# Optimization experiments

Hardware: AMD Instinct MI355X
Metric: run time of the kernel (lower is better)

The kernel has to match this reference:

```python
import jax, jax.numpy as jnp
import numpy as np

N, E = 50000, 800000
NODE_DIM, EDGE_DIM, TIME_DIM, OUT_DIM, N_HEADS = 128, 64, 16, 128, 4
IN_DIM = NODE_DIM + EDGE_DIM + TIME_DIM  # msg_proj input


def setup_inputs() -> dict:
    key = jax.random.key(0)
    ks = jax.random.split(key, 8)
    x = jax.random.normal(ks[0], (N, NODE_DIM), dtype=jnp.float32)
    edge_index = jax.random.randint(ks[1], (2, E), 0, N, dtype=jnp.int32)
    edge_feat = jax.random.normal(ks[2], (E, EDGE_DIM), dtype=jnp.float32)
    time_deltas = jax.random.uniform(ks[3], (E,), dtype=jnp.float32)
    # parameters
    gammas = jnp.ones((TIME_DIM,), jnp.float32)  # ExponentialTimeDecay init_gamma=1.0
    Wm = 0.02 * jax.random.normal(ks[4], (IN_DIM, OUT_DIM), dtype=jnp.float32)
    bm = jnp.zeros((OUT_DIM,), jnp.float32)
    Wa = 0.02 * jax.random.normal(ks[5], (2 * OUT_DIM, N_HEADS), dtype=jnp.float32)
    ba = jnp.zeros((N_HEADS,), jnp.float32)
    Wo = 0.02 * jax.random.normal(ks[6], (OUT_DIM + NODE_DIM, OUT_DIM), dtype=jnp.float32)
    bo = jnp.zeros((OUT_DIM,), jnp.float32)
    ln_g = jnp.ones((OUT_DIM,), jnp.float32)
    ln_b = jnp.zeros((OUT_DIM,), jnp.float32)
    return {"x": x, "edge_index": edge_index, "edge_feat": edge_feat,
            "time_deltas": time_deltas, "gammas": gammas, "Wm": Wm, "bm": bm,
            "Wa": Wa, "ba": ba, "Wo": Wo, "bo": bo, "ln_g": ln_g, "ln_b": ln_b}


def reference(x, edge_index, edge_feat, time_deltas, gammas, Wm, bm, Wa, ba, Wo, bo, ln_g, ln_b):
    src, dst = edge_index[0], edge_index[1]
    # exponential time decay encoding: (E, TIME_DIM)
    dt = jnp.clip(time_deltas, 0.0)[:, None]
    time_enc = jnp.exp(-jax.nn.softplus(gammas)[None, :] * dt)
    # gather + project messages: (E, OUT_DIM)
    msg_in = jnp.concatenate([x[src], edge_feat, time_enc], axis=-1)
    msgs = msg_in @ Wm + bm
    # edge attention, softmax over ALL edges (dim=0, as in the torch code)
    attn_in = jnp.concatenate([msgs, x[dst]], axis=-1)  # (E, 2*OUT_DIM)
    attn_logits = attn_in @ Wa + ba                      # (E, N_HEADS)
    attn_weight = jnp.mean(jax.nn.softmax(attn_logits, axis=0), axis=-1, keepdims=True)
    weighted = msgs * attn_weight
    # scatter-add into per-node aggregates: (N, OUT_DIM)
    agg = jax.ops.segment_sum(weighted, dst, num_segments=N)
    # output MLP (dropout is identity in eval) + LayerNorm
    out = jax.nn.gelu(jnp.concatenate([agg, x], axis=-1) @ Wo + bo, approximate=False)
    mu = jnp.mean(out, axis=-1, keepdims=True)
    var = jnp.mean((out - mu) ** 2, axis=-1, keepdims=True)
    return (out - mu) / jnp.sqrt(var + 1e-5) * ln_g + ln_b
```

## Files before the change

kernel.cpp:

```cpp
#include <hip/hip_runtime.h>
#include <math.h>

#define N_NODES 50000
#define N_EDGES 800000
#define ND 128
#define ED 64
#define TD 16
#define OD 128
#define NH 4
#define INDIM 208
#define K2DIM 336
#define KPAD 352
#define WTPITCH 360
#define NPAD 50048

#define OFF_A      0ll
#define OFF_EXPL   0ll
#define OFF_PERM   8808448ll
#define OFF_DENOM  12008448ll
#define OFF_SPG    12008464ll
#define OFF_WFUSE  12008480ll
#define OFF_BFUSE  12009312ll
#define OFF_BMO    12009328ll
#define OFF_XS4    12009456ll
#define OFF_XD4    12209456ll
#define OFF_CNT    12409456ll
#define OFF_START  12459456ll
#define OFF_CURSOR 12509472ll
#define OFF_SW     12559472ll
#define OFF_WT     12609520ll
#define WS_FLOATS  12632560ll

typedef __attribute__((ext_vector_type(8))) short short8v;
typedef __attribute__((ext_vector_type(4))) float f32x4;

__device__ inline unsigned short f2bf(float f) {
  unsigned u = __float_as_uint(f);
  unsigned r = (u + 0x7fffu + ((u >> 16) & 1u)) >> 16;
  return (unsigned short)r;
}

__global__ void k0_prep(const float* __restrict__ Wm, const float* __restrict__ bm,
                        const float* __restrict__ Wa, const float* __restrict__ ba,
                        const float* __restrict__ Wo, const float* __restrict__ gammas,
                        float* __restrict__ ws) {
  int b = blockIdx.x, j = threadIdx.x;
  unsigned short* Wt = (unsigned short*)(ws + OFF_WT);
  if (b < INDIM) {
    float acc = 0.f;
    for (int m = 0; m < OD; ++m) acc += Wm[b * OD + m] * Wo[m * OD + j];
    Wt[j * WTPITCH + b] = f2bf(acc);
    if (j < NH) {
      float a = 0.f;
      for (int m = 0; m < OD; ++m) a += Wm[b * OD + m] * Wa[m * NH + j];
      ws[OFF_WFUSE + (long)b * NH + j] = a;
    }
  } else if (b < K2DIM) {
    Wt[j * WTPITCH + b] = f2bf(Wo[(OD + b - INDIM) * OD + j]);
  } else {
    if (j < TD) ws[OFF_SPG + j] = log1pf(expf(gammas[j]));
    if (j < NH) {
      float a = ba[j];
      for (int m = 0; m < OD; ++m) a += bm[m] * Wa[m * NH + j];
      ws[OFF_BFUSE + j] = a;
    }
    float a2 = 0.f;
    for (int m = 0; m < OD; ++m) a2 += bm[m] * Wo[m * OD + j];
    ws[OFF_BMO + j] = a2;
    for (int p = K2DIM; p < KPAD; ++p) Wt[j * WTPITCH + p] = 0;
  }
}

__global__ __launch_bounds__(256) void k0b_nodeproj(
    const float* __restrict__ x, const float* __restrict__ Wa,
    float* __restrict__ ws) {
  __shared__ float wf[ND * NH];
  __shared__ float wab[ND * NH];
  int tid = threadIdx.x;
  for (int i = tid; i < ND * NH; i += 256) { wf[i] = ws[OFF_WFUSE + i]; wab[i] = Wa[ND * NH + i]; }
  __syncthreads();
  int lane = tid & 63, wv = tid >> 6;
  long n = (long)blockIdx.x * 4 + wv;
  if (n >= N_NODES) return;
  float v0 = x[n * ND + lane], v1 = x[n * ND + 64 + lane];
  float s0, s1, s2, s3, d0, d1, d2, d3;
  s0 = v0 * wf[lane * 4 + 0] + v1 * wf[(64 + lane) * 4 + 0];
  s1 = v0 * wf[lane * 4 + 1] + v1 * wf[(64 + lane) * 4 + 1];
  s2 = v0 * wf[lane * 4 + 2] + v1 * wf[(64 + lane) * 4 + 2];
  s3 = v0 * wf[lane * 4 + 3] + v1 * wf[(64 + lane) * 4 + 3];
  d0 = v0 * wab[lane * 4 + 0] + v1 * wab[(64 + lane) * 4 + 0];
  d1 = v0 * wab[lane * 4 + 1] + v1 * wab[(64 + lane) * 4 + 1];
  d2 = v0 * wab[lane * 4 + 2] + v1 * wab[(64 + lane) * 4 + 2];
  d3 = v0 * wab[lane * 4 + 3] + v1 * wab[(64 + lane) * 4 + 3];
  for (int off = 32; off; off >>= 1) {
    s0 += __shfl_xor(s0, off); s1 += __shfl_xor(s1, off);
    s2 += __shfl_xor(s2, off); s3 += __shfl_xor(s3, off);
    d0 += __shfl_xor(d0, off); d1 += __shfl_xor(d1, off);
    d2 += __shfl_xor(d2, off); d3 += __shfl_xor(d3, off);
  }
  if (lane == 0) {
    reinterpret_cast<float4*>(ws + OFF_XS4)[n] = make_float4(s0, s1, s2, s3);
    reinterpret_cast<float4*>(ws + OFF_XD4)[n] = make_float4(d0, d1, d2, d3);
  }
}

__global__ __launch_bounds__(256) void k1_logits(
    const int* __restrict__ ei, const float* __restrict__ ef,
    const float* __restrict__ td, float* __restrict__ ws) {
  __shared__ float wef[ED * NH];
  __shared__ float wte[TD * NH];
  __shared__ float bf[NH];
  __shared__ float spg[TD];
  __shared__ float part[NH];
  int tid = threadIdx.x;
  for (int i = tid; i < ED * NH; i += 256) wef[i] = ws[OFF_WFUSE + ND * NH + i];
  if (tid < TD * NH) wte[tid] = ws[OFF_WFUSE + (ND + ED) * NH + tid];
  if (tid < NH) { bf[tid] = ws[OFF_BFUSE + tid]; part[tid] = 0.f; }
  if (tid < TD) spg[tid] = ws[OFF_SPG + tid];
  __syncthreads();

  int r = tid & 15;
  long grp = ((long)blockIdx.x * 256 + tid) >> 4;
  long ngrp = ((long)gridDim.x * 256) >> 4;
  const float4* ef4 = reinterpret_cast<const float4*>(ef);
  float4* expl4 = reinterpret_cast<float4*>(ws + OFF_EXPL);
  const float4* xs4 = reinterpret_cast<const float4*>(ws + OFF_XS4);
  const float4* xd4 = reinterpret_cast<const float4*>(ws + OFF_XD4);
  int* cnt = reinterpret_cast<int*>(ws + OFF_CNT);
  float p0 = 0.f, p1 = 0.f, p2 = 0.f, p3 = 0.f;

  for (long e = grp; e < N_EDGES; e += ngrp) {
    float4 efv = ef4[e * 16 + r];
    const float* w0 = &wef[(4 * r) * 4];
    float a0 = efv.x * w0[0] + efv.y * w0[4] + efv.z * w0[8]  + efv.w * w0[12];
    float a1 = efv.x * w0[1] + efv.y * w0[5] + efv.z * w0[9]  + efv.w * w0[13];
    float a2 = efv.x * w0[2] + efv.y * w0[6] + efv.z * w0[10] + efv.w * w0[14];
    float a3 = efv.x * w0[3] + efv.y * w0[7] + efv.z * w0[11] + efv.w * w0[15];
    float dt = fmaxf(td[e], 0.f);
    float te = expf(-spg[r] * dt);
    a0 += te * wte[r * 4 + 0]; a1 += te * wte[r * 4 + 1];
    a2 += te * wte[r * 4 + 2]; a3 += te * wte[r * 4 + 3];
    for (int off = 8; off; off >>= 1) {
      a0 += __shfl_xor(a0, off); a1 += __shfl_xor(a1, off);
      a2 += __shfl_xor(a2, off); a3 += __shfl_xor(a3, off);
    }
    if (r == 0) {
      int s = ei[e], d = ei[N_EDGES + e];
      float4 xs = xs4[s], xd = xd4[d];
      float e0 = expf(a0 + xs.x + xd.x + bf[0]);
      float e1 = expf(a1 + xs.y + xd.y + bf[1]);
      float e2 = expf(a2 + xs.z + xd.z + bf[2]);
      float e3 = expf(a3 + xs.w + xd.w + bf[3]);
      expl4[e] = make_float4(e0, e1, e2, e3);
      p0 += e0; p1 += e1; p2 += e2; p3 += e3;
      atomicAdd(&cnt[d], 1);
    }
  }
  if ((tid & 15) == 0) {
    atomicAdd(&part[0], p0); atomicAdd(&part[1], p1);
    atomicAdd(&part[2], p2); atomicAdd(&part[3], p3);
  }
  __syncthreads();
  if (tid < NH) atomicAdd(&ws[OFF_DENOM + tid], part[tid]);
}

__global__ __launch_bounds__(1024) void k_scan(float* __restrict__ ws) {
  const int* cnt = reinterpret_cast<const int*>(ws + OFF_CNT);
  int* startp = reinterpret_cast<int*>(ws + OFF_START);
  int* cursor = reinterpret_cast<int*>(ws + OFF_CURSOR);
  __shared__ int wsum[16];
  int tid = threadIdx.x;
  int lo = tid * 49, hi = min(lo + 49, N_NODES);
  int s = 0;
  for (int i = lo; i < hi; ++i) s += cnt[i];
  int lane = tid & 63, wv = tid >> 6;
  int sc = s;
  for (int off = 1; off < 64; off <<= 1) {
    int t = __shfl_up(sc, off);
    if (lane >= off) sc += t;
  }
  if (lane == 63) wsum[wv] = sc;
  __syncthreads();
  if (tid == 0) {
    int run = 0;
    for (int i = 0; i < 16; ++i) { int t = wsum[i]; wsum[i] = run; run += t; }
  }
  __syncthreads();
  int run = wsum[wv] + sc - s;
  for (int i = lo; i < hi; ++i) { startp[i] = run; cursor[i] = run; run += cnt[i]; }
  if (tid == 1023) startp[N_NODES] = run;
}

__global__ __launch_bounds__(256) void k_fill(const int* __restrict__ ei,
                                              const float* __restrict__ td,
                                              float* __restrict__ ws) {
  __shared__ float inv[NH];
  int tid = threadIdx.x;
  if (tid < NH) inv[tid] = 0.25f / ws[OFF_DENOM + tid];
  __syncthreads();
  const float4* expl4 = reinterpret_cast<const float4*>(ws + OFF_EXPL);
  int* cursor = reinterpret_cast<int*>(ws + OFF_CURSOR);
  uint4* perm = reinterpret_cast<uint4*>(ws + OFF_PERM);
  for (long e = (long)blockIdx.x * 256 + tid; e < N_EDGES; e += (long)gridDim.x * 256) {
    int s = ei[e], d = ei[N_EDGES + e];
    float4 ev = expl4[e];
    float w = ev.x * inv[0] + ev.y * inv[1] + ev.z * inv[2] + ev.w * inv[3];
    float dt = fmaxf(td[e], 0.f);
    int pos = atomicAdd(&cursor[d], 1);
    perm[pos] = make_uint4((unsigned)s, (unsigned)e, __float_as_uint(w), __float_as_uint(dt));
  }
}

__global__ __launch_bounds__(256) void k4a_agg(
    const float* __restrict__ x, const float* __restrict__ ef,
    float* __restrict__ ws) {
  __shared__ float spg_s[TD];
  int tid = threadIdx.x;
  if (tid < TD) spg_s[tid] = ws[OFF_SPG + tid];
  __syncthreads();
  int lane = tid & 63;
  long wid = (long)blockIdx.x * 4 + (tid >> 6);
  long nw = (long)gridDim.x * 4;
  const int* start = reinterpret_cast<const int*>(ws + OFF_START);
  const uint4* perm = reinterpret_cast<const uint4*>(ws + OFF_PERM);
  unsigned short* A = (unsigned short*)(ws + OFF_A);
  float spg_l = spg_s[lane & 15];

  for (long n = wid; n < N_NODES; n += nw) {
    int i0 = start[n], i1 = start[n + 1];
    float a0 = 0.f, a1 = 0.f, a2 = 0.f, a3 = 0.f, asw = 0.f;
    for (int base = i0; base < i1; base += 64) {
      int m = min(64, i1 - base);
      uint4 pk = make_uint4(0u, 0u, 0u, 0u);
      if (lane < m) pk = perm[base + lane];
      for (int j = 0; j < m; ++j) {
        int s  = __shfl((int)pk.x, j);
        int e  = __shfl((int)pk.y, j);
        float w  = __uint_as_float(__shfl((int)pk.z, j));
        float dt = __uint_as_float(__shfl((int)pk.w, j));
        a0 += w * x[(long)s * ND + lane];
        a1 += w * x[(long)s * ND + 64 + lane];
        a2 += w * ef[(long)e * ED + lane];
        a3 += w * __expf(-spg_l * dt);
        asw += w;
      }
    }
    unsigned short* Ar = A + n * KPAD;
    float xv0 = x[n * ND + lane], xv1 = x[n * ND + 64 + lane];
    Ar[lane] = f2bf(a0);
    Ar[64 + lane] = f2bf(a1);
    Ar[128 + lane] = f2bf(a2);
    if (lane < TD) Ar[192 + lane] = f2bf(a3);
    Ar[INDIM + lane] = f2bf(xv0);
    Ar[INDIM + 64 + lane] = f2bf(xv1);
    if (lane < 16) Ar[K2DIM + lane] = 0;
    if (lane == 0) ws[OFF_SW + n] = asw;
  }
}

__global__ __launch_bounds__(256) void k4b_mlp(
    const float* __restrict__ bo, const float* __restrict__ lng,
    const float* __restrict__ lnb, const float* __restrict__ ws,
    float* __restrict__ out) {
  __shared__ unsigned short wt[128 * WTPITCH];
  __shared__ float tbl[512];
  int tid = threadIdx.x;
  {
    const unsigned* wg = (const unsigned*)(ws + OFF_WT);
    unsigned* wl = (unsigned*)wt;
    for (int i = tid; i < 128 * WTPITCH / 2; i += 256) wl[i] = wg[i];
    if (tid < 128) {
      tbl[tid] = bo[tid];
      tbl[128 + tid] = ws[OFF_BMO + tid];
      tbl[256 + tid] = lng[tid];
      tbl[384 + tid] = lnb[tid];
    }
  }
  __syncthreads();

  int lane = tid & 63, wv = tid >> 6;
  int c0 = lane & 15, grp = lane >> 4;
  long n0 = (long)blockIdx.x * 64 + (long)wv * 16;
  const unsigned short* A = (const unsigned short*)(ws + OFF_A);
  const unsigned short* Arow = A + (n0 + c0) * KPAD;

  f32x4 acc[8];
#pragma unroll
  for (int t = 0; t < 8; ++t) acc[t] = (f32x4){0.f, 0.f, 0.f, 0.f};

#pragma unroll
  for (int kt = 0; kt < 11; ++kt) {
    short8v afrag = *reinterpret_cast<const short8v*>(Arow + kt * 32 + grp * 8);
#pragma unroll
    for (int t = 0; t < 8; ++t) {
      short8v bfrag = *reinterpret_cast<const short8v*>(&wt[(t * 16 + c0) * WTPITCH + kt * 32 + grp * 8]);
      acc[t] = __builtin_amdgcn_mfma_f32_16x16x32_bf16(afrag, bfrag, acc[t], 0, 0, 0);
    }
  }

  const float* swp = ws + OFF_SW;
  float res[4][8];
#pragma unroll
  for (int r = 0; r < 4; ++r) {
    long row = n0 + grp * 4 + r;
    float sw = swp[row];
    float s = 0.f, s2 = 0.f;
#pragma unroll
    for (int t = 0; t < 8; ++t) {
      int col = c0 + 16 * t;
      float a = acc[t][r] + tbl[col] + sw * tbl[128 + col];
      float h = 0.5f * a * (1.f + erff(a * 0.70710678118654752f));
      res[r][t] = h;
      s += h; s2 += h * h;
    }
    s += __shfl_xor(s, 1);  s2 += __shfl_xor(s2, 1);
    s += __shfl_xor(s, 2);  s2 += __shfl_xor(s2, 2);
    s += __shfl_xor(s, 4);  s2 += __shfl_xor(s2, 4);
    s += __shfl_xor(s, 8);  s2 += __shfl_xor(s2, 8);
    float mu = s * (1.f / 128.f);
    float var = s2 * (1.f / 128.f) - mu * mu;
    float rstd = rsqrtf(var + 1e-5f);
    if (row < N_NODES) {
      float* op = out + row * OD;
#pragma unroll
      for (int t = 0; t < 8; ++t) {
        int col = c0 + 16 * t;
        op[col] = (res[r][t] - mu) * rstd * tbl[256 + col] + tbl[384 + col];
      }
    }
  }
}

extern "C" void kernel_launch(void* const* d_in, const int* in_sizes, int n_in,
                              void* d_out, int out_size, void* d_ws, size_t ws_size,
                              hipStream_t stream) {
  const float* x   = (const float*)d_in[0];
  const int*   ei  = (const int*)d_in[1];
  const float* ef  = (const float*)d_in[2];
  const float* td  = (const float*)d_in[3];
  const float* gm  = (const float*)d_in[4];
  const float* Wm  = (const float*)d_in[5];
  const float* bm  = (const float*)d_in[6];
  const float* Wa  = (const float*)d_in[7];
  const float* ba  = (const float*)d_in[8];
  const float* Wo  = (const float*)d_in[9];
  const float* bo  = (const float*)d_in[10];
  const float* lng = (const float*)d_in[11];
  const float* lnb = (const float*)d_in[12];
  float* ws = (float*)d_ws;
  float* out = (float*)d_out;
  if (ws_size < (size_t)WS_FLOATS * 4) return;

  hipMemsetAsync(ws + OFF_CNT, 0, 50000 * 4, stream);
  hipMemsetAsync(ws + OFF_DENOM, 0, 64, stream);

  k0_prep<<<K2DIM + 1, 128, 0, stream>>>(Wm, bm, Wa, ba, Wo, gm, ws);
  k0b_nodeproj<<<12500, 256, 0, stream>>>(x, Wa, ws);
  k1_logits<<<1024, 256, 0, stream>>>(ei, ef, td, ws);
  k_scan<<<1, 1024, 0, stream>>>(ws);
  k_fill<<<1024, 256, 0, stream>>>(ei, td, ws);
  k4a_agg<<<2048, 256, 0, stream>>>(x, ef, ws);
  k4b_mlp<<<(NPAD / 64), 256, 0, stream>>>(bo, lng, lnb, ws, out);
}
```

Baseline: 455.3 us.

## Restructure edge logits to 4 edges per wave and batch gather loads

The logits kernel now handles four edges per 64-lane wave, with weights held in registers. Every lane does useful work: it issues its own index, time and node-projection loads and uses a transposed shuffle reduction instead of the 16-lane butterfly with a single active writer. The aggregation loop is unrolled by four so the independent x and edge-feature gathers can be in flight together, raising memory-level parallelism. Grid sizes for the logits and fill kernels are doubled. The cost is higher register pressure and the use of the approximate __expf in the logits kernel.

```diff
diff --git a/kernel.cpp b/kernel.cpp
--- a/kernel.cpp
+++ b/kernel.cpp
@@ -119,47 +119,54 @@
   if (tid < TD) spg[tid] = ws[OFF_SPG + tid];
   __syncthreads();
 
-  int r = tid & 15;
-  long grp = ((long)blockIdx.x * 256 + tid) >> 4;
-  long ngrp = ((long)gridDim.x * 256) >> 4;
+  int lane = tid & 63;
+  int q = lane >> 4, r = lane & 15, h = r & 3;
+  long wid = ((long)blockIdx.x * 256 + tid) >> 6;
+  long stride = (long)gridDim.x * 16;
   const float4* ef4 = reinterpret_cast<const float4*>(ef);
-  float4* expl4 = reinterpret_cast<float4*>(ws + OFF_EXPL);
-  const float4* xs4 = reinterpret_cast<const float4*>(ws + OFF_XS4);
-  const float4* xd4 = reinterpret_cast<const float4*>(ws + OFF_XD4);
+  float* expl = ws + OFF_EXPL;
+  const float* xsf = ws + OFF_XS4;
+  const float* xdf = ws + OFF_XD4;
   int* cnt = reinterpret_cast<int*>(ws + OFF_CNT);
-  float p0 = 0.f, p1 = 0.f, p2 = 0.f, p3 = 0.f;
-
-  for (long e = grp; e < N_EDGES; e += ngrp) {
+
+  float wr[16];
+#pragma unroll
+  for (int i = 0; i < 16; ++i) wr[i] = wef[16 * r + i];
+  float spg_r = spg[r];
+  float wt0 = wte[r * 4 + 0], wt1 = wte[r * 4 + 1];
+  float wt2 = wte[r * 4 + 2], wt3 = wte[r * 4 + 3];
+  float bfh = bf[h];
+  float p = 0.f;
+
+  for (long e = wid * 4 + q; e < N_EDGES; e += stride) {
+    int s = ei[e];
+    int d = ei[N_EDGES + e];
+    float dt = fmaxf(td[e], 0.f);
     float4 efv = ef4[e * 16 + r];
-    const float* w0 = &wef[(4 * r) * 4];
-    float a0 = efv.x * w0[0] + efv.y * w0[4] + efv.z * w0[8]  + efv.w * w0[12];
-    float a1 = efv.x * w0[1] + efv.y * w0[5] + efv.z * w0[9]  + efv.w * w0[13];
-    float a2 = efv.x * w0[2] + efv.y * w0[6] + efv.z * w0[10] + efv.w * w0[14];
-    float a3 = efv.x * w0[3] + efv.y * w0[7] + efv.z * w0[11] + efv.w * w0[15];
-    float dt = fmaxf(td[e], 0.f);
-    float te = expf(-spg[r] * dt);
-    a0 += te * wte[r * 4 + 0]; a1 += te * wte[r * 4 + 1];
-    a2 += te * wte[r * 4 + 2]; a3 += te * wte[r * 4 + 3];
-    for (int off = 8; off; off >>= 1) {
-      a0 += __shfl_xor(a0, off); a1 += __shfl_xor(a1, off);
-      a2 += __shfl_xor(a2, off); a3 += __shfl_xor(a3, off);
-    }
-    if (r == 0) {
-      int s = ei[e], d = ei[N_EDGES + e];
-      float4 xs = xs4[s], xd = xd4[d];
-      float e0 = expf(a0 + xs.x + xd.x + bf[0]);
-      float e1 = expf(a1 + xs.y + xd.y + bf[1]);
-      float e2 = expf(a2 + xs.z + xd.z + bf[2]);
-      float e3 = expf(a3 + xs.w + xd.w + bf[3]);
-      expl4[e] = make_float4(e0, e1, e2, e3);
-      p0 += e0; p1 += e1; p2 += e2; p3 += e3;
-      atomicAdd(&cnt[d], 1);
-    }
-  }
-  if ((tid & 15) == 0) {
-    atomicAdd(&part[0], p0); atomicAdd(&part[1], p1);
-    atomicAdd(&part[2], p2); atomicAdd(&part[3], p3);
-  }
+    float ls = xsf[4l * s + h];
+    float ld = xdf[4l * d + h];
+    float te = __expf(-spg_r * dt);
+    float a0 = efv.x * wr[0] + efv.y * wr[4] + efv.z * wr[8]  + efv.w * wr[12] + te * wt0;
+    float a1 = efv.x * wr[1] + efv.y * wr[5] + efv.z * wr[9]  + efv.w * wr[13] + te * wt1;
+    float a2 = efv.x * wr[2] + efv.y * wr[6] + efv.z * wr[10] + efv.w * wr[14] + te * wt2;
+    float a3 = efv.x * wr[3] + efv.y * wr[7] + efv.z * wr[11] + efv.w * wr[15] + te * wt3;
+    a0 += __shfl_xor(a0, 1); a1 += __shfl_xor(a1, 1);
+    a2 += __shfl_xor(a2, 1); a3 += __shfl_xor(a3, 1);
+    a0 += __shfl_xor(a0, 2); a1 += __shfl_xor(a1, 2);
+    a2 += __shfl_xor(a2, 2); a3 += __shfl_xor(a3, 2);
+    float v = a0;
+    v = (h == 1) ? a1 : v;
+    v = (h == 2) ? a2 : v;
+    v = (h == 3) ? a3 : v;
+    v += __shfl_xor(v, 4);
+    v += __shfl_xor(v, 8);
+    float ev = __expf(v + ls + ld + bfh);
+    if (r < 4) { expl[e * 4 + r] = ev; p += ev; }
+    if (r == 1) atomicAdd(&cnt[d], 1);
+  }
+  p += __shfl_xor(p, 16);
+  p += __shfl_xor(p, 32);
+  if (lane < 4) atomicAdd(&part[lane], p);
   __syncthreads();
   if (tid < NH) atomicAdd(&ws[OFF_DENOM + tid], part[tid]);
 }
@@ -233,7 +240,33 @@
       int m = min(64, i1 - base);
       uint4 pk = make_uint4(0u, 0u, 0u, 0u);
       if (lane < m) pk = perm[base + lane];
-      for (int j = 0; j < m; ++j) {
+      int j = 0;
+      for (; j + 4 <= m; j += 4) {
+        int s4[4], e4[4]; float w4[4], dt4[4];
+#pragma unroll
+        for (int u = 0; u < 4; ++u) {
+          s4[u]  = __shfl((int)pk.x, j + u);
+          e4[u]  = __shfl((int)pk.y, j + u);
+          w4[u]  = __uint_as_float(__shfl((int)pk.z, j + u));
+          dt4[u] = __uint_as_float(__shfl((int)pk.w, j + u));
+        }
+        float xa[4], xb[4], ec[4];
+#pragma unroll
+        for (int u = 0; u < 4; ++u) {
+          xa[u] = x[(long)s4[u] * ND + lane];
+          xb[u] = x[(long)s4[u] * ND + 64 + lane];
+          ec[u] = ef[(long)e4[u] * ED + lane];
+        }
+#pragma unroll
+        for (int u = 0; u < 4; ++u) {
+          a0 += w4[u] * xa[u];
+          a1 += w4[u] * xb[u];
+          a2 += w4[u] * ec[u];
+          a3 += w4[u] * __expf(-spg_l * dt4[u]);
+          asw += w4[u];
+        }
+      }
+      for (; j < m; ++j) {
         int s  = __shfl((int)pk.x, j);
         int e  = __shfl((int)pk.y, j);
         float w  = __uint_as_float(__shfl((int)pk.z, j));
@@ -356,9 +389,9 @@
 
   k0_prep<<<K2DIM + 1, 128, 0, stream>>>(Wm, bm, Wa, ba, Wo, gm, ws);
   k0b_nodeproj<<<12500, 256, 0, stream>>>(x, Wa, ws);
-  k1_logits<<<1024, 256, 0, stream>>>(ei, ef, td, ws);
+  k1_logits<<<2048, 256, 0, stream>>>(ei, ef, td, ws);
   k_scan<<<1, 1024, 0, stream>>>(ws);
-  k_fill<<<1024, 256, 0, stream>>>(ei, td, ws);
+  k_fill<<<2048, 256, 0, stream>>>(ei, td, ws);
   k4a_agg<<<2048, 256, 0, stream>>>(x, ef, ws);
   k4b_mlp<<<(NPAD / 64), 256, 0, stream>>>(bo, lng, lnb, ws, out);
 }
```

Result: faster. 432.0 us (-5.1%).
